# Kernel tuning notes

Hardware: AMD Instinct MI355X
Metric: run time of the kernel (lower is better)

Reference implementation:

```python
import jax, jax.numpy as jnp
import numpy as np

GROUPS = [16, 16, 32, 64, 192]
B, H, W = 8, 64, 64


def _shift(x, dy, dx):
    # out[i, j] = x[i - dy, j - dx], zero padded (equiv. of PoolConv's depthwise shift convs)
    Hh, Ww = x.shape[-2], x.shape[-1]
    pt, pb = max(dy, 0), max(-dy, 0)
    pl, pr = max(dx, 0), max(-dx, 0)
    xp = jnp.pad(x, ((0, 0), (0, 0), (pt, pb), (pl, pr)))
    return xp[..., pb:pb + Hh, pr:pr + Ww]


def _conv5(x, w, b):
    out = jax.lax.conv_general_dilated(x, w, (1, 1), ((2, 2), (2, 2)),
                                       dimension_numbers=("NCHW", "OIHW", "NCHW"))
    return out + b[None, :, None, None]


def _fill_pool(x, m1):
    # bottom: w[0,0]=1, pad 1 -> shift down-right; top: w[2,0]=1 -> shift up-right; right: w[2,0] of 5x5, pad 2 -> shift right by 2
    xm = x * m1
    return x + _shift(xm, 1, 1) + _shift(xm, -1, 1) + _shift(xm, 0, 2)


def _forward(y, mask, sws, sbs, cws, cbs):
    m0, m1 = mask[0], mask[1]
    starts = np.cumsum([0] + GROUPS[:-1])
    outs = []
    prev = None
    for i, g in enumerate(GROUPS):
        s = y[:, int(starts[i]):int(starts[i]) + g]
        anchor = _fill_pool(s * m0, m1)
        sp = _conv5(anchor, sws[i], sbs[i]) * (1.0 - m0)
        if i == 0:
            outs.append(sp)
            prev = s
        else:
            ch = _conv5(prev, cws[i - 1], cbs[i - 1])
            outs.append(sp)
            outs.append(ch)
            prev = jnp.concatenate([prev, s], axis=1)
    return tuple(outs)


def setup_inputs() -> dict:
    key = jax.random.key(0)
    ks = jax.random.split(key, 32)
    y = jax.random.normal(ks[0], (B, sum(GROUPS), H, W), jnp.float32)
    hh, ww = jnp.meshgrid(jnp.arange(H), jnp.arange(W), indexing="ij")
    m0 = (((hh + ww) % 2) == 0).astype(jnp.float32)[None, None]  # checkerboard anchor mask
    mask = jnp.stack([m0, 1.0 - m0], axis=0)  # [2,1,1,H,W]
    starts = np.cumsum([0] + GROUPS[:-1])
    inp = {"y": y, "mask": mask, "stage": 1}
    for i, g in enumerate(GROUPS):
        inp[f"sw{i}"] = 0.02 * jax.random.normal(ks[1 + i], (2 * g, g, 5, 5), jnp.float32)
        inp[f"sb{i}"] = jnp.zeros((2 * g,), jnp.float32)
    for i in range(1, len(GROUPS)):
        inp[f"cw{i}"] = 0.02 * jax.random.normal(ks[10 + i], (2 * GROUPS[i], int(starts[i]), 5, 5), jnp.float32)
        inp[f"cb{i}"] = jnp.zeros((2 * GROUPS[i],), jnp.float32)
    return inp


def reference(y, mask, stage, sw0, sb0, sw1, sb1, sw2, sb2, sw3, sb3, sw4, sb4,
              cw1, cb1, cw2, cb2, cw3, cb3, cw4, cb4):
    # stage != TRAIN branch: AdaptiveContext returns only the conv output
    return _forward(y, mask,
                    [sw0, sw1, sw2, sw3, sw4], [sb0, sb1, sb2, sb3, sb4],
                    [cw1, cw2, cw3, cw4], [cb1, cb2, cb3, cb4])
```

## Files before the change

### kernel.cpp

```cpp
#include <hip/hip_runtime.h>

typedef __bf16 bf16_t;
typedef __bf16 bf16x8 __attribute__((ext_vector_type(8)));
typedef float f32x16 __attribute__((ext_vector_type(16)));

#define CTOT 320
#define NPIX 32768

#define SPLANE_U 6544
#define SPLANE_M 5776
#define SWOFF    13088

__global__ __launch_bounds__(256) void k_transpose_y(const float* __restrict__ y,
                                                     bf16_t* __restrict__ yt,
                                                     bf16_t* __restrict__ ytp) {
  __shared__ bf16_t T[64][72];
  int blk = blockIdx.x;
  int c0 = (blk % 5) * 64;
  int bh = blk / 5;
  int b = bh >> 6, h = bh & 63;
  int tid = threadIdx.x;
  {
    int c = tid >> 2, w0 = (tid & 3) << 4;
    const float* src = y + (size_t)(b * CTOT + c0 + c) * 4096 + (h << 6) + w0;
#pragma unroll
    for (int j = 0; j < 16; j += 4) {
      float4 v = *(const float4*)(src + j);
      T[c][w0 + j + 0] = (bf16_t)v.x;
      T[c][w0 + j + 1] = (bf16_t)v.y;
      T[c][w0 + j + 2] = (bf16_t)v.z;
      T[c][w0 + j + 3] = (bf16_t)v.w;
    }
  }
  __syncthreads();
  {
    int w = tid >> 2, cq = (tid & 3) << 4;
    union { uint4 v; bf16_t b[8]; } u0, u1;
#pragma unroll
    for (int j = 0; j < 8; ++j) { u0.b[j] = T[cq + j][w]; u1.b[j] = T[cq + 8 + j][w]; }
    bf16_t* dst = yt + (size_t)((bh << 6) | w) * CTOT + c0 + cq;
    *(uint4*)dst = u0.v;
    *(uint4*)(dst + 8) = u1.v;
  }
  if (tid < 128) {
    int j = tid >> 2, cq = (tid & 3) << 4;
    int w = (j << 1) + (h & 1);
    union { uint4 v; bf16_t b[8]; } u0, u1;
#pragma unroll
    for (int k = 0; k < 8; ++k) { u0.b[k] = T[cq + k][w]; u1.b[k] = T[cq + 8 + k][w]; }
    bf16_t* dst = ytp + (size_t)((bh << 5) + j) * CTOT + c0 + cq;
    *(uint4*)dst = u0.v;
    *(uint4*)(dst + 8) = u1.v;
  }
}

__global__ __launch_bounds__(256) void k_transpose_w(const float* __restrict__ w,
                                                     bf16_t* __restrict__ wt,
                                                     int IC, int OC, int OCp) {
  int idx = blockIdx.x * 256 + threadIdx.x;
  if (idx >= OCp * IC) return;
  int oc = idx / IC, ic = idx - oc * IC;
  bool valid = (oc < OC);
  const float* src = w + (size_t)(oc * IC + ic) * 25;
#pragma unroll
  for (int t = 0; t < 25; ++t) {
    float v = valid ? src[t] : 0.0f;
    wt[(size_t)(t * OCp + oc) * IC + ic] = (bf16_t)v;
  }
}

struct ConvDesc {
  const float* bias;
  int out_off, wt_off;
  int ICp, OC, OCp, chs, masked, job_start;
};
struct MainParams {
  const bf16_t* yt;
  const bf16_t* ytp;
  const bf16_t* wt;
  float* out;
  ConvDesc cv[9];
};

template <bool MASKED>
__device__ __forceinline__ void conv_run(const ConvDesc cd, const MainParams& P,
                                         int local, bf16_t* S) {
  constexpr int NT = MASKED ? 12 : 25;
  constexpr int SPLANE = MASKED ? SPLANE_M : SPLANE_U;
  int mb = MASKED ? (local >> 5) : (local >> 6);
  int nb = local & (MASKED ? 31 : 63);
  int b  = MASKED ? (nb >> 2) : (nb >> 3);
  int hblk = MASKED ? ((nb & 3) << 4) : ((nb & 7) << 3);
  int tid = threadIdx.x;
  int lane = tid & 63, wn = tid >> 6;
  int l31 = lane & 31, kq = lane >> 5;

  int octmax = (cd.OC - (mb << 6)) >> 5; if (octmax > 2) octmax = 2;

  f32x16 acc00 = {}, acc01 = {}, acc10 = {}, acc11 = {};

  int aoff = SWOFF + kq * 512 + l31 * 8;
  int boff = MASKED ? (kq * SPLANE_M + ((wn << 1) * 36 + 1 + l31) * 8)
                    : (kq * SPLANE_U + (wn * 68 + l31) * 8);

  const bf16_t* wtc = P.wt + cd.wt_off;
  int nchunks = cd.ICp >> 4;

  for (int cb = 0; cb < nchunks; ++cb) {
    int ic0 = cb << 4;
    if (cb) __syncthreads();
    if (!MASKED) {
      for (int t = tid; t < 1632; t += 512) {
        int rr = t / 136, rem = t - rr * 136;
        int cc = rem >> 1, icg = rem & 1;
        int h = hblk + rr - 2, w = cc - 2;
        uint4 v = {0u, 0u, 0u, 0u};
        if (((unsigned)h < 64u) && ((unsigned)w < 64u))
          v = *(const uint4*)(P.yt + (size_t)((((b << 6) + h) << 6) | w) * CTOT + cd.chs + ic0 + (icg << 3));
        *(uint4*)(S + icg * SPLANE_U + (rr * 68 + cc) * 8) = v;
      }
    } else {
      for (int t = tid; t < 1360; t += 512) {
        int rr = t / 68, rem = t - rr * 68;
        int cc = rem >> 1, icg = rem & 1;
        int h = hblk + rr - 2, j = cc - 1;
        uint4 v = {0u, 0u, 0u, 0u};
        if (((unsigned)h < 64u) && ((unsigned)j < 32u))
          v = *(const uint4*)(P.ytp + (size_t)((((b << 6) + h) << 5) + j) * CTOT + cd.chs + ic0 + (icg << 3));
        *(uint4*)(S + icg * SPLANE_M + (rr * 36 + cc) * 8) = v;
      }
    }
    for (int t = tid; t < NT * 128; t += 512) {
      int ti = t >> 7, rem = t & 127;
      int oc = rem >> 1, icg = rem & 1;
      int tap = MASKED ? (2 * ti + 1) : ti;
      int wo = (tap * cd.OCp + (mb << 6) + oc) * cd.ICp + ic0 + (icg << 3);
      *(uint4*)(S + SWOFF + ti * 1024 + icg * 512 + oc * 8) = *(const uint4*)(wtc + wo);
    }
    __syncthreads();

#pragma unroll
    for (int it = 0; it < NT; ++it) {
      int tap = MASKED ? (2 * it + 1) : it;
      int dy = tap / 5, dx = tap - dy * 5;
      bf16x8 af0 = *(const bf16x8*)(S + aoff + it * 1024);
      bf16x8 bf0, bf1;
      if (!MASKED) {
        int toff = (dy * 68 + dx) * 8;
        bf0 = *(const bf16x8*)(S + boff + toff);
        bf1 = *(const bf16x8*)(S + boff + toff + 256);
      } else {
        int j0 = (1 + dx - 2 - (dy & 1)) / 2;
        int j1 = (dx - 2 - ((dy + 1) & 1)) / 2;
        bf0 = *(const bf16x8*)(S + boff + (dy * 36 + j0) * 8);
        bf1 = *(const bf16x8*)(S + boff + ((dy + 1) * 36 + j1) * 8);
      }
      acc00 = __builtin_amdgcn_mfma_f32_32x32x16_bf16(af0, bf0, acc00, 0, 0, 0);
      acc01 = __builtin_amdgcn_mfma_f32_32x32x16_bf16(af0, bf1, acc01, 0, 0, 0);
      if (octmax > 1) {
        bf16x8 af1 = *(const bf16x8*)(S + aoff + it * 1024 + 256);
        acc10 = __builtin_amdgcn_mfma_f32_32x32x16_bf16(af1, bf0, acc10, 0, 0, 0);
        acc11 = __builtin_amdgcn_mfma_f32_32x32x16_bf16(af1, bf1, acc11, 0, 0, 0);
      }
    }
  }

  float* outp = P.out + cd.out_off;
#define EPI_U(A, OT, PT)                                                        \
  {                                                                             \
    int h = hblk + wn;                                                          \
    _Pragma("unroll")                                                           \
    for (int r = 0; r < 16; ++r) {                                              \
      int row = (r & 3) + ((r >> 2) << 3) + (kq << 2);                          \
      int oc = (mb << 6) + ((OT) << 5) + row;                                   \
      outp[(size_t)(b * cd.OC + oc) * 4096 + (h << 6) + ((PT) << 5) + l31] =    \
          (A)[r] + cd.bias[oc];                                                 \
    }                                                                           \
  }
#define EPI_M(A, OT, PT)                                                        \
  {                                                                             \
    int h = hblk + (wn << 1) + (PT);                                            \
    _Pragma("unroll")                                                           \
    for (int r = 0; r < 16; ++r) {                                              \
      int row = (r & 3) + ((r >> 2) << 3) + (kq << 2);                          \
      int oc = (mb << 6) + ((OT) << 5) + row;                                   \
      float val = (A)[r] + cd.bias[oc];                                         \
      float2 pr;                                                                \
      if ((PT) == 0) { pr.x = 0.0f; pr.y = val; }                               \
      else           { pr.x = val;  pr.y = 0.0f; }                              \
      *(float2*)(outp + (size_t)(b * cd.OC + oc) * 4096 + (h << 6) + (l31 << 1)) = pr; \
    }                                                                           \
  }
  if (!MASKED) {
    EPI_U(acc00, 0, 0); EPI_U(acc01, 0, 1);
    if (octmax > 1) { EPI_U(acc10, 1, 0); EPI_U(acc11, 1, 1); }
  } else {
    EPI_M(acc00, 0, 0); EPI_M(acc01, 0, 1);
    if (octmax > 1) { EPI_M(acc10, 1, 0); EPI_M(acc11, 1, 1); }
  }
#undef EPI_U
#undef EPI_M
}

__global__ __launch_bounds__(512, 4) void k_conv_main(MainParams P) {
  __shared__ bf16_t S[38688];
  int bid = blockIdx.x;
  int ci = 0;
#pragma unroll
  for (int i = 1; i < 9; ++i) if (bid >= P.cv[i].job_start) ci = i;
  ConvDesc cd = P.cv[ci];
  int local = bid - cd.job_start;
  if (cd.masked) conv_run<true>(cd, P, local, S);
  else           conv_run<false>(cd, P, local, S);
}

extern "C" void kernel_launch(void* const* d_in, const int* in_sizes, int n_in,
                              void* d_out, int out_size, void* d_ws, size_t ws_size,
                              hipStream_t stream) {
  const float* y = (const float*)d_in[0];
  bf16_t* yt  = (bf16_t*)d_ws;
  bf16_t* ytp = yt + (size_t)NPIX * CTOT;
  bf16_t* wt  = ytp + (size_t)(NPIX / 2) * CTOT;

  k_transpose_y<<<2560, 256, 0, stream>>>(y, yt, ytp);

  static const int ICv[9]  = {128,    192,    64,     32,     16,     64,     32,     16,    16};
  static const int OCv[9]  = {384,    384,    128,    64,     32,     128,    64,     32,    32};
  static const int OCp[9]  = {384,    384,    128,    64,     64,     128,    64,     64,    64};
  static const int WIDX[9] = {19,     11,     17,     15,     13,     9,      7,      5,     3};
  static const int BIDX[9] = {20,     12,     18,     16,     14,     10,     8,      6,     4};
  static const int CHS[9]  = {0,      128,    0,      0,      0,      64,     32,     16,    0};
  static const int MSK[9]  = {0,      1,      0,      0,      0,      1,      1,      1,     1};
  static const int WTOFF[9] = {0, 1228800, 3072000, 3276800, 3328000,
                               3353600, 3558400, 3609600, 3635200};
  static const int OUTOFF[9] = {28311552, 15728640, 11534336, 5242880, 2097152,
                                7340032,  3145728,  1048576,  0};
  static const int JOBST[9] = {0, 384, 576, 704, 768, 832, 896, 928, 960};

  for (int i = 0; i < 9; ++i) {
    int n = OCp[i] * ICv[i];
    k_transpose_w<<<(n + 255) / 256, 256, 0, stream>>>(
        (const float*)d_in[WIDX[i]], wt + WTOFF[i], ICv[i], OCv[i], OCp[i]);
  }

  MainParams P;
  P.yt = yt; P.ytp = ytp; P.wt = wt; P.out = (float*)d_out;
  for (int i = 0; i < 9; ++i) {
    P.cv[i].bias = (const float*)d_in[BIDX[i]];
    P.cv[i].out_off = OUTOFF[i];
    P.cv[i].wt_off = WTOFF[i];
    P.cv[i].ICp = ICv[i]; P.cv[i].OC = OCv[i]; P.cv[i].OCp = OCp[i];
    P.cv[i].chs = CHS[i]; P.cv[i].masked = MSK[i];
    P.cv[i].job_start = JOBST[i];
  }
  k_conv_main<<<992, 512, 0, stream>>>(P);
}
```

Baseline: 196.8 us.

## Register-prefetch conv inputs and split tap weights into two LDS halves

After: 307.6 us. 1.56x slower.

```diff
diff --git a/kernel.cpp b/kernel.cpp
--- a/kernel.cpp
+++ b/kernel.cpp
@@ -9,7 +9,6 @@
 
 #define SPLANE_U 6544
 #define SPLANE_M 5776
-#define SWOFF    13088
 
 __global__ __launch_bounds__(256) void k_transpose_y(const float* __restrict__ y,
                                                      bf16_t* __restrict__ yt,
@@ -85,8 +84,15 @@
 template <bool MASKED>
 __device__ __forceinline__ void conv_run(const ConvDesc cd, const MainParams& P,
                                          int local, bf16_t* S) {
-  constexpr int NT = MASKED ? 12 : 25;
-  constexpr int SPLANE = MASKED ? SPLANE_M : SPLANE_U;
+  constexpr int NT  = MASKED ? 12 : 25;
+  constexpr int NTA = MASKED ? 6 : 13;
+  constexpr int NTB = NT - NTA;
+  constexpr int SWOFF_T = 2 * (MASKED ? SPLANE_M : SPLANE_U);
+  constexpr int NSIN = MASKED ? 1360 : 1632;
+  constexpr int ISIN = (NSIN + 511) / 512;
+  constexpr int ISWA = (NTA * 128 + 511) / 512;
+  constexpr int ISWB = (NTB * 128 + 511) / 512;
+
   int mb = MASKED ? (local >> 5) : (local >> 6);
   int nb = local & (MASKED ? 31 : 63);
   int b  = MASKED ? (nb >> 2) : (nb >> 3);
@@ -99,71 +105,140 @@
 
   f32x16 acc00 = {}, acc01 = {}, acc10 = {}, acc11 = {};
 
-  int aoff = SWOFF + kq * 512 + l31 * 8;
+  int aoff = SWOFF_T + kq * 512 + l31 * 8;
   int boff = MASKED ? (kq * SPLANE_M + ((wn << 1) * 36 + 1 + l31) * 8)
                     : (kq * SPLANE_U + (wn * 68 + l31) * 8);
 
   const bf16_t* wtc = P.wt + cd.wt_off;
   int nchunks = cd.ICp >> 4;
 
+  uint4 rin[ISIN], rwa[ISWA], rwb[ISWB];
+
+  auto sin_task = [&](int t, int& dst, const bf16_t*& src, bool& inb) {
+    if (!MASKED) {
+      int rr = t / 136, rem = t - rr * 136, cc = rem >> 1, icg = rem & 1;
+      int h = hblk + rr - 2, w = cc - 2;
+      inb = (((unsigned)h < 64u) & ((unsigned)w < 64u)) != 0;
+      dst = icg * SPLANE_U + (rr * 68 + cc) * 8;
+      int hh = inb ? h : 0, ww = inb ? w : 0;
+      src = P.yt + (size_t)((((b << 6) + hh) << 6) | ww) * CTOT + cd.chs + (icg << 3);
+    } else {
+      int rr = t / 68, rem = t - rr * 68, cc = rem >> 1, icg = rem & 1;
+      int h = hblk + rr - 2, j = cc - 1;
+      inb = (((unsigned)h < 64u) & ((unsigned)j < 32u)) != 0;
+      dst = icg * SPLANE_M + (rr * 36 + cc) * 8;
+      int hh = inb ? h : 0, jj = inb ? j : 0;
+      src = P.ytp + (size_t)((((b << 6) + hh) << 5) + jj) * CTOT + cd.chs + (icg << 3);
+    }
+  };
+  auto sw_task = [&](int t, bool grpB, int& dst, int& srcoff) {
+    int slot = t >> 7, rem = t & 127, oc = rem >> 1, icg = rem & 1;
+    int tidx = slot + (grpB ? NTA : 0);
+    int tap = MASKED ? (2 * tidx + 1) : tidx;
+    dst = SWOFF_T + slot * 1024 + icg * 512 + oc * 8;
+    srcoff = (tap * cd.OCp + (mb << 6) + oc) * cd.ICp + (icg << 3);
+  };
+
+  auto issue_sina = [&](int ic0) {
+#pragma unroll
+    for (int i = 0; i < ISIN; ++i) {
+      int t = i * 512 + tid;
+      bool tv = (t < NSIN);
+      int dst; const bf16_t* src; bool inb;
+      sin_task(tv ? t : 0, dst, src, inb);
+      if (tv && inb) rin[i] = *(const uint4*)(src + ic0);
+    }
+#pragma unroll
+    for (int i = 0; i < ISWA; ++i) {
+      int t = i * 512 + tid;
+      bool tv = (t < NTA * 128);
+      int dst, srcoff;
+      sw_task(tv ? t : 0, false, dst, srcoff);
+      if (tv) rwa[i] = *(const uint4*)(wtc + srcoff + ic0);
+    }
+  };
+  auto commit_sina = [&]() {
+    const uint4 z = {0u, 0u, 0u, 0u};
+#pragma unroll
+    for (int i = 0; i < ISIN; ++i) {
+      int t = i * 512 + tid;
+      bool tv = (t < NSIN);
+      int dst; const bf16_t* src; bool inb;
+      sin_task(tv ? t : 0, dst, src, inb);
+      if (tv) *(uint4*)(S + dst) = inb ? rin[i] : z;
+    }
+#pragma unroll
+    for (int i = 0; i < ISWA; ++i) {
+      int t = i * 512 + tid;
+      bool tv = (t < NTA * 128);
+      int dst, srcoff;
+      sw_task(tv ? t : 0, false, dst, srcoff);
+      if (tv) *(uint4*)(S + dst) = rwa[i];
+    }
+  };
+  auto issue_b = [&](int ic0) {
+#pragma unroll
+    for (int i = 0; i < ISWB; ++i) {
+      int t = i * 512 + tid;
+      bool tv = (t < NTB * 128);
+      int dst, srcoff;
+      sw_task(tv ? t : 0, true, dst, srcoff);
+      if (tv) rwb[i] = *(const uint4*)(wtc + srcoff + ic0);
+    }
+  };
+  auto commit_b = [&]() {
+#pragma unroll
+    for (int i = 0; i < ISWB; ++i) {
+      int t = i * 512 + tid;
+      bool tv = (t < NTB * 128);
+      int dst, srcoff;
+      sw_task(tv ? t : 0, true, dst, srcoff);
+      if (tv) *(uint4*)(S + dst) = rwb[i];
+    }
+  };
+
+#define TAP_ONE(S_, TAPIDX)                                                     \
+  {                                                                             \
+    int tap_ = MASKED ? (2 * (TAPIDX) + 1) : (TAPIDX);                          \
+    int dy_ = tap_ / 5, dx_ = tap_ % 5;                                         \
+    bf16x8 af0 = *(const bf16x8*)(S + aoff + (S_) * 1024);                      \
+    bf16x8 bf0, bf1;                                                            \
+    if (!MASKED) {                                                              \
+      int toff_ = (dy_ * 68 + dx_) * 8;                                         \
+      bf0 = *(const bf16x8*)(S + boff + toff_);                                 \
+      bf1 = *(const bf16x8*)(S + boff + toff_ + 256);                           \
+    } else {                                                                    \
+      int j0_ = (dx_ - 1 - (dy_ & 1)) / 2;                                      \
+      int j1_ = (dx_ - 2 - ((dy_ + 1) & 1)) / 2;                                \
+      bf0 = *(const bf16x8*)(S + boff + (dy_ * 36 + j0_) * 8);                  \
+      bf1 = *(const bf16x8*)(S + boff + ((dy_ + 1) * 36 + j1_) * 8);            \
+    }                                                                           \
+    acc00 = __builtin_amdgcn_mfma_f32_32x32x16_bf16(af0, bf0, acc00, 0, 0, 0);  \
+    acc01 = __builtin_amdgcn_mfma_f32_32x32x16_bf16(af0, bf1, acc01, 0, 0, 0);  \
+    if (octmax > 1) {                                                           \
+      bf16x8 af1 = *(const bf16x8*)(S + aoff + (S_) * 1024 + 256);              \
+      acc10 = __builtin_amdgcn_mfma_f32_32x32x16_bf16(af1, bf0, acc10, 0, 0, 0);\
+      acc11 = __builtin_amdgcn_mfma_f32_32x32x16_bf16(af1, bf1, acc11, 0, 0, 0);\
+    }                                                                           \
+  }
+
+  issue_sina(0);
   for (int cb = 0; cb < nchunks; ++cb) {
     int ic0 = cb << 4;
     if (cb) __syncthreads();
-    if (!MASKED) {
-      for (int t = tid; t < 1632; t += 512) {
-        int rr = t / 136, rem = t - rr * 136;
-        int cc = rem >> 1, icg = rem & 1;
-        int h = hblk + rr - 2, w = cc - 2;
-        uint4 v = {0u, 0u, 0u, 0u};
-        if (((unsigned)h < 64u) && ((unsigned)w < 64u))
-          v = *(const uint4*)(P.yt + (size_t)((((b << 6) + h) << 6) | w) * CTOT + cd.chs + ic0 + (icg << 3));
-        *(uint4*)(S + icg * SPLANE_U + (rr * 68 + cc) * 8) = v;
-      }
-    } else {
-      for (int t = tid; t < 1360; t += 512) {
-        int rr = t / 68, rem = t - rr * 68;
-        int cc = rem >> 1, icg = rem & 1;
-        int h = hblk + rr - 2, j = cc - 1;
-        uint4 v = {0u, 0u, 0u, 0u};
-        if (((unsigned)h < 64u) && ((unsigned)j < 32u))
-          v = *(const uint4*)(P.ytp + (size_t)((((b << 6) + h) << 5) + j) * CTOT + cd.chs + ic0 + (icg << 3));
-        *(uint4*)(S + icg * SPLANE_M + (rr * 36 + cc) * 8) = v;
-      }
-    }
-    for (int t = tid; t < NT * 128; t += 512) {
-      int ti = t >> 7, rem = t & 127;
-      int oc = rem >> 1, icg = rem & 1;
-      int tap = MASKED ? (2 * ti + 1) : ti;
-      int wo = (tap * cd.OCp + (mb << 6) + oc) * cd.ICp + ic0 + (icg << 3);
-      *(uint4*)(S + SWOFF + ti * 1024 + icg * 512 + oc * 8) = *(const uint4*)(wtc + wo);
-    }
+    commit_sina();
     __syncthreads();
-
-#pragma unroll
-    for (int it = 0; it < NT; ++it) {
-      int tap = MASKED ? (2 * it + 1) : it;
-      int dy = tap / 5, dx = tap - dy * 5;
-      bf16x8 af0 = *(const bf16x8*)(S + aoff + it * 1024);
-      bf16x8 bf0, bf1;
-      if (!MASKED) {
-        int toff = (dy * 68 + dx) * 8;
-        bf0 = *(const bf16x8*)(S + boff + toff);
-        bf1 = *(const bf16x8*)(S + boff + toff + 256);
-      } else {
-        int j0 = (1 + dx - 2 - (dy & 1)) / 2;
-        int j1 = (dx - 2 - ((dy + 1) & 1)) / 2;
-        bf0 = *(const bf16x8*)(S + boff + (dy * 36 + j0) * 8);
-        bf1 = *(const bf16x8*)(S + boff + ((dy + 1) * 36 + j1) * 8);
-      }
-      acc00 = __builtin_amdgcn_mfma_f32_32x32x16_bf16(af0, bf0, acc00, 0, 0, 0);
-      acc01 = __builtin_amdgcn_mfma_f32_32x32x16_bf16(af0, bf1, acc01, 0, 0, 0);
-      if (octmax > 1) {
-        bf16x8 af1 = *(const bf16x8*)(S + aoff + it * 1024 + 256);
-        acc10 = __builtin_amdgcn_mfma_f32_32x32x16_bf16(af1, bf0, acc10, 0, 0, 0);
-        acc11 = __builtin_amdgcn_mfma_f32_32x32x16_bf16(af1, bf1, acc11, 0, 0, 0);
-      }
-    }
-  }
+    issue_b(ic0);
+#pragma unroll
+    for (int s = 0; s < NTA; ++s) TAP_ONE(s, s);
+    __syncthreads();
+    commit_b();
+    __syncthreads();
+    if (cb + 1 < nchunks) issue_sina(ic0 + 16);
+#pragma unroll
+    for (int s = 0; s < NTB; ++s) TAP_ONE(s, s + NTA);
+  }
+#undef TAP_ONE
 
   float* outp = P.out + cd.out_off;
 #define EPI_U(A, OT, PT)                                                        \
@@ -203,7 +278,7 @@
 }
 
 __global__ __launch_bounds__(512, 4) void k_conv_main(MainParams P) {
-  __shared__ bf16_t S[38688];
+  __shared__ bf16_t S[26400];
   int bid = blockIdx.x;
   int ci = 0;
 #pragma unroll
```

## Double-buffer conv staging with direct global-to-LDS loads and regrouped weight layout

Applied to the files above, without the earlier changes.

After: 207.1 us. +5.3%, slower.

```diff
diff --git a/kernel.cpp b/kernel.cpp
--- a/kernel.cpp
+++ b/kernel.cpp
@@ -3,13 +3,15 @@
 typedef __bf16 bf16_t;
 typedef __bf16 bf16x8 __attribute__((ext_vector_type(8)));
 typedef float f32x16 __attribute__((ext_vector_type(16)));
+typedef unsigned int u32;
 
 #define CTOT 320
 #define NPIX 32768
 
-#define SPLANE_U 6544
-#define SPLANE_M 5776
-#define SWOFF    13088
+__device__ __forceinline__ void gload16(const void* g, void* l) {
+  __builtin_amdgcn_global_load_lds((const __attribute__((address_space(1))) u32*)g,
+                                   (__attribute__((address_space(3))) u32*)l, 16, 0, 0);
+}
 
 __global__ __launch_bounds__(256) void k_transpose_y(const float* __restrict__ y,
                                                      bf16_t* __restrict__ yt,
@@ -62,12 +64,15 @@
   int oc = idx / IC, ic = idx - oc * IC;
   bool valid = (oc < OC);
   const float* src = w + (size_t)(oc * IC + ic) * 25;
+  int icg = ic >> 3, ie = ic & 7;
 #pragma unroll
   for (int t = 0; t < 25; ++t) {
     float v = valid ? src[t] : 0.0f;
-    wt[(size_t)(t * OCp + oc) * IC + ic] = (bf16_t)v;
-  }
-}
+    wt[(size_t)((t * (IC >> 3) + icg) * OCp + oc) * 8 + ie] = (bf16_t)v;
+  }
+}
+
+__global__ void k_zero(uint4* z) { z[threadIdx.x] = uint4{0u, 0u, 0u, 0u}; }
 
 struct ConvDesc {
   const float* bias;
@@ -78,6 +83,7 @@
   const bf16_t* yt;
   const bf16_t* ytp;
   const bf16_t* wt;
+  const bf16_t* zp;
   float* out;
   ConvDesc cv[9];
 };
@@ -85,90 +91,106 @@
 template <bool MASKED>
 __device__ __forceinline__ void conv_run(const ConvDesc cd, const MainParams& P,
                                          int local, bf16_t* S) {
-  constexpr int NT = MASKED ? 12 : 25;
-  constexpr int SPLANE = MASKED ? SPLANE_M : SPLANE_U;
+  constexpr int NT   = MASKED ? 12 : 25;
+  constexpr int COLS = MASKED ? 36 : 68;
+  constexpr int REAL = MASKED ? 720 : 816;
+  constexpr int NSG  = MASKED ? 12 : 13;
+  constexpr int SPL  = NSG * 512;
+  constexpr int SWO  = 2 * SPL;
+  constexpr int BUFSZ = SWO + NT * 1024;
+
   int mb = MASKED ? (local >> 5) : (local >> 6);
   int nb = local & (MASKED ? 31 : 63);
   int b  = MASKED ? (nb >> 2) : (nb >> 3);
   int hblk = MASKED ? ((nb & 3) << 4) : ((nb & 7) << 3);
-  int tid = threadIdx.x;
-  int lane = tid & 63, wn = tid >> 6;
+  int tid = threadIdx.x, lane = tid & 63, wid = tid >> 6;
   int l31 = lane & 31, kq = lane >> 5;
 
   int octmax = (cd.OC - (mb << 6)) >> 5; if (octmax > 2) octmax = 2;
 
   f32x16 acc00 = {}, acc01 = {}, acc10 = {}, acc11 = {};
 
-  int aoff = SWOFF + kq * 512 + l31 * 8;
-  int boff = MASKED ? (kq * SPLANE_M + ((wn << 1) * 36 + 1 + l31) * 8)
-                    : (kq * SPLANE_U + (wn * 68 + l31) * 8);
+  int aofs = SWO + kq * 512 + l31 * 8;
+  int bofs = kq * SPL + (MASKED ? (((wid << 1) * 36 + 1 + l31) * 8)
+                                : ((wid * 68 + l31) * 8));
 
   const bf16_t* wtc = P.wt + cd.wt_off;
+  int icgs = cd.ICp >> 3;
   int nchunks = cd.ICp >> 4;
 
+  auto stage = [&](int cb, int buf) {
+    int ic0 = cb << 4;
+    bf16_t* Sb = S + buf * BUFSZ;
+    for (int g = wid; g < 2 * NSG; g += 8) {
+      int p = (g >= NSG) ? 1 : 0;
+      int gi = g - p * NSG;
+      int s = (gi << 6) + lane;
+      int rr = s / COLS, cc = s - rr * COLS;
+      int h = hblk + rr - 2;
+      const bf16_t* gp;
+      if (!MASKED) {
+        int w = cc - 2;
+        bool inb = (s < REAL) && ((unsigned)h < 64u) && ((unsigned)w < 64u);
+        gp = inb ? (P.yt + (size_t)((((b << 6) + (h & 63)) << 6) | (w & 63)) * CTOT
+                        + cd.chs + ic0 + (p << 3))
+                 : P.zp;
+      } else {
+        int j = cc - 1;
+        bool inb = (s < REAL) && ((unsigned)h < 64u) && ((unsigned)j < 32u);
+        gp = inb ? (P.ytp + (size_t)((((b << 6) + (h & 63)) << 5) + (j & 31)) * CTOT
+                         + cd.chs + ic0 + (p << 3))
+                 : P.zp;
+      }
+      gload16(gp, Sb + p * SPL + (gi << 9));
+    }
+    for (int g = wid; g < 2 * NT; g += 8) {
+      int slot = g >> 1, icg = g & 1;
+      int tap = MASKED ? (2 * slot + 1) : slot;
+      const bf16_t* gp = wtc +
+          (size_t)((tap * icgs + (ic0 >> 3) + icg) * cd.OCp + (mb << 6) + lane) * 8;
+      gload16(gp, Sb + SWO + (g << 9));
+    }
+  };
+
+  stage(0, 0);
   for (int cb = 0; cb < nchunks; ++cb) {
-    int ic0 = cb << 4;
-    if (cb) __syncthreads();
-    if (!MASKED) {
-      for (int t = tid; t < 1632; t += 512) {
-        int rr = t / 136, rem = t - rr * 136;
-        int cc = rem >> 1, icg = rem & 1;
-        int h = hblk + rr - 2, w = cc - 2;
-        uint4 v = {0u, 0u, 0u, 0u};
-        if (((unsigned)h < 64u) && ((unsigned)w < 64u))
-          v = *(const uint4*)(P.yt + (size_t)((((b << 6) + h) << 6) | w) * CTOT + cd.chs + ic0 + (icg << 3));
-        *(uint4*)(S + icg * SPLANE_U + (rr * 68 + cc) * 8) = v;
-      }
-    } else {
-      for (int t = tid; t < 1360; t += 512) {
-        int rr = t / 68, rem = t - rr * 68;
-        int cc = rem >> 1, icg = rem & 1;
-        int h = hblk + rr - 2, j = cc - 1;
-        uint4 v = {0u, 0u, 0u, 0u};
-        if (((unsigned)h < 64u) && ((unsigned)j < 32u))
-          v = *(const uint4*)(P.ytp + (size_t)((((b << 6) + h) << 5) + j) * CTOT + cd.chs + ic0 + (icg << 3));
-        *(uint4*)(S + icg * SPLANE_M + (rr * 36 + cc) * 8) = v;
-      }
-    }
-    for (int t = tid; t < NT * 128; t += 512) {
-      int ti = t >> 7, rem = t & 127;
-      int oc = rem >> 1, icg = rem & 1;
-      int tap = MASKED ? (2 * ti + 1) : ti;
-      int wo = (tap * cd.OCp + (mb << 6) + oc) * cd.ICp + ic0 + (icg << 3);
-      *(uint4*)(S + SWOFF + ti * 1024 + icg * 512 + oc * 8) = *(const uint4*)(wtc + wo);
-    }
     __syncthreads();
-
-#pragma unroll
-    for (int it = 0; it < NT; ++it) {
-      int tap = MASKED ? (2 * it + 1) : it;
-      int dy = tap / 5, dx = tap - dy * 5;
-      bf16x8 af0 = *(const bf16x8*)(S + aoff + it * 1024);
-      bf16x8 bf0, bf1;
-      if (!MASKED) {
-        int toff = (dy * 68 + dx) * 8;
-        bf0 = *(const bf16x8*)(S + boff + toff);
-        bf1 = *(const bf16x8*)(S + boff + toff + 256);
-      } else {
-        int j0 = (1 + dx - 2 - (dy & 1)) / 2;
-        int j1 = (dx - 2 - ((dy + 1) & 1)) / 2;
-        bf0 = *(const bf16x8*)(S + boff + (dy * 36 + j0) * 8);
-        bf1 = *(const bf16x8*)(S + boff + ((dy + 1) * 36 + j1) * 8);
-      }
-      acc00 = __builtin_amdgcn_mfma_f32_32x32x16_bf16(af0, bf0, acc00, 0, 0, 0);
-      acc01 = __builtin_amdgcn_mfma_f32_32x32x16_bf16(af0, bf1, acc01, 0, 0, 0);
-      if (octmax > 1) {
-        bf16x8 af1 = *(const bf16x8*)(S + aoff + it * 1024 + 256);
-        acc10 = __builtin_amdgcn_mfma_f32_32x32x16_bf16(af1, bf0, acc10, 0, 0, 0);
-        acc11 = __builtin_amdgcn_mfma_f32_32x32x16_bf16(af1, bf1, acc11, 0, 0, 0);
-      }
-    }
+    if (cb + 1 < nchunks) stage(cb + 1, (cb + 1) & 1);
+    const bf16_t* Sb = S + (cb & 1) * BUFSZ;
+
+#define TAP_ONE(TI)                                                             \
+    {                                                                           \
+      int tap_ = MASKED ? (2 * (TI) + 1) : (TI);                                \
+      int dy_ = tap_ / 5, dx_ = tap_ % 5;                                       \
+      bf16x8 af0 = *(const bf16x8*)(Sb + aofs + (TI) * 1024);                   \
+      bf16x8 bf0, bf1;                                                          \
+      if (!MASKED) {                                                            \
+        int toff_ = (dy_ * 68 + dx_) * 8;                                       \
+        bf0 = *(const bf16x8*)(Sb + bofs + toff_);                              \
+        bf1 = *(const bf16x8*)(Sb + bofs + toff_ + 256);                        \
+      } else {                                                                  \
+        int j0_ = (dx_ - 1 - (dy_ & 1)) / 2;                                    \
+        int j1_ = (dx_ - 2 - ((dy_ + 1) & 1)) / 2;                              \
+        bf0 = *(const bf16x8*)(Sb + bofs + (dy_ * 36 + j0_) * 8);               \
+        bf1 = *(const bf16x8*)(Sb + bofs + ((dy_ + 1) * 36 + j1_) * 8);         \
+      }                                                                         \
+      acc00 = __builtin_amdgcn_mfma_f32_32x32x16_bf16(af0, bf0, acc00, 0, 0, 0);\
+      acc01 = __builtin_amdgcn_mfma_f32_32x32x16_bf16(af0, bf1, acc01, 0, 0, 0);\
+      if (octmax > 1) {                                                         \
+        bf16x8 af1 = *(const bf16x8*)(Sb + aofs + (TI) * 1024 + 256);           \
+        acc10 = __builtin_amdgcn_mfma_f32_32x32x16_bf16(af1, bf0, acc10, 0,0,0);\
+        acc11 = __builtin_amdgcn_mfma_f32_32x32x16_bf16(af1, bf1, acc11, 0,0,0);\
+      }                                                                         \
+    }
+#pragma unroll
+    for (int s = 0; s < NT; ++s) TAP_ONE(s)
+#undef TAP_ONE
   }
 
   float* outp = P.out + cd.out_off;
 #define EPI_U(A, OT, PT)                                                        \
   {                                                                             \
-    int h = hblk + wn;                                                          \
+    int h = hblk + wid;                                                         \
     _Pragma("unroll")                                                           \
     for (int r = 0; r < 16; ++r) {                                              \
       int row = (r & 3) + ((r >> 2) << 3) + (kq << 2);                          \
@@ -179,7 +201,7 @@
   }
 #define EPI_M(A, OT, PT)                                                        \
   {                                                                             \
-    int h = hblk + (wn << 1) + (PT);                                            \
+    int h = hblk + (wid << 1) + (PT);                                           \
     _Pragma("unroll")                                                           \
     for (int r = 0; r < 16; ++r) {                                              \
       int row = (r & 3) + ((r >> 2) << 3) + (kq << 2);                          \
@@ -202,8 +224,8 @@
 #undef EPI_M
 }
 
-__global__ __launch_bounds__(512, 4) void k_conv_main(MainParams P) {
-  __shared__ bf16_t S[38688];
+__global__ __launch_bounds__(512, 2) void k_conv_main(MainParams P) {
+  __shared__ bf16_t S[77824];
   int bid = blockIdx.x;
   int ci = 0;
 #pragma unroll
@@ -221,8 +243,10 @@
   bf16_t* yt  = (bf16_t*)d_ws;
   bf16_t* ytp = yt + (size_t)NPIX * CTOT;
   bf16_t* wt  = ytp + (size_t)(NPIX / 2) * CTOT;
+  bf16_t* zp  = wt + 3660800;
 
   k_transpose_y<<<2560, 256, 0, stream>>>(y, yt, ytp);
+  k_zero<<<1, 64, 0, stream>>>((uint4*)zp);
 
   static const int ICv[9]  = {128,    192,    64,     32,     16,     64,     32,     16,    16};
   static const int OCv[9]  = {384,    384,    128,    64,     32,     128,    64,     32,    32};
@@ -244,7 +268,7 @@
   }
 
   MainParams P;
-  P.yt = yt; P.ytp = ytp; P.wt = wt; P.out = (float*)d_out;
+  P.yt = yt; P.ytp = ytp; P.wt = wt; P.zp = zp; P.out = (float*)d_out;
   for (int i = 0; i < 9; ++i) {
     P.cv[i].bias = (const float*)d_in[BIDX[i]];
     P.cv[i].out_off = OUTOFF[i];
```
